# Performance work log

Measured on AMD Instinct MI355X. Metric: run time of the kernel, lower is better.

The kernel has to match this reference:

```python
import jax, jax.numpy as jnp
import numpy as np

M_BLEND = 0.3
LR_REFINE = 0.1
N_REFINE = 10
N_SAMPLES = 256
USE_INFONCE = True
MARGIN = 0.2
TAU = 0.07


def safe_norm(x, eps=1e-8):
    return x / jnp.maximum(jnp.linalg.norm(x, axis=-1, keepdims=True), eps)


def setup_inputs() -> dict:
    key = jax.random.key(0)
    k1, k2, k3, k4 = jax.random.split(key, 4)
    fg_proto = safe_norm(jax.random.normal(k1, (64, 512), dtype=jnp.float32))
    bg_proto = safe_norm(jax.random.normal(k2, (64, 512), dtype=jnp.float32))
    F_map = jax.random.normal(k3, (16, 512, 96, 96), dtype=jnp.float32)
    M_map = jax.random.uniform(k4, (16, 96, 96), dtype=jnp.float32)
    return {"fg_proto": fg_proto, "bg_proto": bg_proto, "F_map": F_map, "M_map": M_map}


def _refine(feats, protos):
    # iterative k-means-like refinement: argmax assign -> per-cluster mean -> blended, renormalized centroid
    p = protos
    K = p.shape[0]
    ones = jnp.ones((feats.shape[0],), feats.dtype)
    for it in range(N_REFINE):
        step = LR_REFINE / (1.0 + 0.5 * it)
        assign = jnp.argmax(feats @ p.T, axis=1)                      # [S]
        sums = jax.ops.segment_sum(feats, assign, num_segments=K)    # [K, C]
        counts = jax.ops.segment_sum(ones, assign, num_segments=K)   # [K]
        cluster_mean = sums / jnp.maximum(counts, 1.0)[:, None]
        new_p = safe_norm((1.0 - step) * p + step * cluster_mean)
        p = jnp.where((counts > 0)[:, None], new_p, p)                # only update non-empty clusters
    return p


def reference(fg_proto, bg_proto, F_map, M_map):
    N, C, H, W = F_map.shape
    # M_map already at (H, W): nearest interpolation is identity; clamp to [0, 1]
    M_flat = jnp.clip(M_map.reshape(-1), 0.0, 1.0)                    # [N*H*W]
    F_flat = safe_norm(F_map.transpose(0, 2, 3, 1).reshape(-1, C))    # [N*H*W, C]

    sim_fg = F_flat @ fg_proto.T                                      # [P, Kf]
    sim_bg = F_flat @ bg_proto.T                                      # [P, Kb]
    dist_fg_min = 1.0 - sim_fg.max(axis=1)
    dist_bg_min = 1.0 - sim_bg.max(axis=1)

    k = min(N_SAMPLES, F_flat.shape[0])
    score_fg = jax.lax.stop_gradient(dist_fg_min * M_flat)
    score_bg = jax.lax.stop_gradient(dist_bg_min * (1.0 - M_flat))
    pos_idx = jax.lax.top_k(score_fg, k)[1]
    neg_idx = jax.lax.top_k(score_bg, k)[1]

    # refinement runs under no_grad in the original
    F_sg = jax.lax.stop_gradient(F_flat)
    p_fg = _refine(F_sg[pos_idx], jax.lax.stop_gradient(fg_proto))
    p_bg = _refine(F_sg[neg_idx], jax.lax.stop_gradient(bg_proto))

    # triplet loss (note: sim_neg also uses p_fg, as in the original)
    pos_feats = safe_norm(F_flat[pos_idx])
    neg_feats = safe_norm(F_flat[neg_idx])
    sim_pos = (pos_feats @ p_fg.T).max(axis=1).mean()
    sim_neg = (neg_feats @ p_fg.T).max(axis=1).mean()
    loss = jax.nn.relu(MARGIN + sim_neg - sim_pos)

    if USE_INFONCE:
        pos_sim = pos_feats @ p_fg.T / TAU                            # [k, Kf]
        neg_sim = pos_feats @ p_bg.T / TAU                            # [k, Kb]
        numerator = jax.scipy.special.logsumexp(pos_sim, axis=1)
        denominator = jax.scipy.special.logsumexp(jnp.concatenate([pos_sim, neg_sim], axis=1), axis=1)
        loss = loss + 0.25 * (-(numerator - denominator).mean())

    refined_fg = safe_norm((1.0 - M_BLEND) * fg_proto + M_BLEND * p_fg)
    refined_bg = safe_norm((1.0 - M_BLEND) * bg_proto + M_BLEND * p_bg)
    return loss, refined_fg, refined_bg
```

## Files before the change

kernel.cpp:

```cpp
#include <hip/hip_runtime.h>
#include <math.h>

#define P_TOTAL 147456
#define HW 9216
#define CHW (512*9216)
#define C_DIM 512
#define KP 64

__device__ __forceinline__ unsigned f2key(float f) {
    unsigned u = __float_as_uint(f);
    return (u & 0x80000000u) ? ~u : (u | 0x80000000u);
}

__global__ void k_init(const float* __restrict__ fg, const float* __restrict__ bg,
                       float* __restrict__ protoT, float* __restrict__ pwork) {
    int i = blockIdx.x * 256 + threadIdx.x;
    int side = i >> 15;
    int r = i & 32767;
    int k = r >> 9;
    int c = r & 511;
    float v = (side ? bg : fg)[k * 512 + c];
    protoT[side * 32768 + c * 64 + k] = v;
    pwork[side * 32768 + k * 512 + c] = v;
}

__global__ __launch_bounds__(256) void k_score(const float* __restrict__ F,
                                               const float* __restrict__ protoT,
                                               float* __restrict__ md_fg,
                                               float* __restrict__ md_bg,
                                               float* __restrict__ n2out) {
    __shared__ float lds[2048];
    const int side = blockIdx.y;
    const int p = blockIdx.x * 256 + threadIdx.x;
    const int n = p / HW;
    const int hw = p - n * HW;
    const float* Fp = F + (size_t)n * CHW + hw;
    const float* PT = protoT + side * (C_DIM * 64);

    float acc[64];
#pragma unroll
    for (int k = 0; k < 64; ++k) acc[k] = 0.f;
    float n2 = 0.f;

    for (int cc = 0; cc < 16; ++cc) {
        __syncthreads();
#pragma unroll
        for (int i = 0; i < 8; ++i)
            lds[threadIdx.x + 256 * i] = PT[cc * 2048 + threadIdx.x + 256 * i];
        __syncthreads();
        for (int c = 0; c < 32; ++c) {
            float f = Fp[(size_t)(cc * 32 + c) * HW];
            if (side == 0) n2 = fmaf(f, f, n2);
#pragma unroll
            for (int k = 0; k < 64; ++k) acc[k] = fmaf(f, lds[c * 64 + k], acc[k]);
        }
    }
    float m = acc[0];
#pragma unroll
    for (int k = 1; k < 64; ++k) m = fmaxf(m, acc[k]);
    if (side == 0) { md_fg[p] = m; n2out[p] = n2; }
    else          { md_bg[p] = m; }
}

__global__ void k_combine(const float* __restrict__ M,
                          float* __restrict__ sfg, float* __restrict__ sbg,
                          float* __restrict__ n2inv) {
    int p = blockIdx.x * 256 + threadIdx.x;
    float inv = 1.f / fmaxf(sqrtf(n2inv[p]), 1e-8f);
    float m = fminf(fmaxf(M[p], 0.f), 1.f);
    float sf = (1.f - sfg[p] * inv) * m;
    float sb = (1.f - sbg[p] * inv) * (1.f - m);
    sfg[p] = sf; sbg[p] = sb; n2inv[p] = inv;
}

__global__ void k_hist1(const float* __restrict__ sfg, const float* __restrict__ sbg,
                        unsigned* __restrict__ hist) {
    int side = blockIdx.y;
    int p = blockIdx.x * 256 + threadIdx.x;
    float s = side ? sbg[p] : sfg[p];
    atomicAdd(&hist[side * 65536 + (f2key(s) >> 16)], 1u);
}

__global__ void k_hist2(const float* __restrict__ sfg, const float* __restrict__ sbg,
                        const int* __restrict__ ctrl, unsigned* __restrict__ hist2) {
    int side = blockIdx.y;
    int p = blockIdx.x * 256 + threadIdx.x;
    float s = side ? sbg[p] : sfg[p];
    unsigned key = f2key(s);
    if ((int)(key >> 16) == ctrl[side * 8 + 0])
        atomicAdd(&hist2[side * 65536 + (key & 0xffffu)], 1u);
}

__global__ __launch_bounds__(1024) void k_scan(const unsigned* __restrict__ hist,
                                               int* __restrict__ ctrl, int pass) {
    __shared__ unsigned sd[1024];
    int side = blockIdx.x;
    const unsigned* h = hist + side * 65536;
    int t = threadIdx.x;
    unsigned partial = 0;
    for (int j = 0; j < 64; ++j) partial += h[65535 - (t * 64 + j)];
    sd[t] = partial;
    __syncthreads();
    for (int off = 1; off < 1024; off <<= 1) {
        unsigned v = (t >= off) ? sd[t - off] : 0u;
        __syncthreads();
        sd[t] += v;
        __syncthreads();
    }
    unsigned incl = sd[t];
    unsigned excl = incl - partial;
    unsigned target = (pass == 0) ? 256u : (unsigned)ctrl[side * 8 + 1];
    if (excl < target && target <= incl) {
        unsigned cum = excl;
        for (int j = 0; j < 64; ++j) {
            int b = 65535 - (t * 64 + j);
            unsigned c = h[b];
            if (cum + c >= target) {
                if (pass == 0) {
                    ctrl[side * 8 + 0] = b;
                    ctrl[side * 8 + 1] = (int)(target - cum);
                } else {
                    unsigned vkey = ((unsigned)ctrl[side * 8 + 0] << 16) | (unsigned)b;
                    ctrl[side * 8 + 2] = (int)vkey;
                    int n_gt = (int)(256u - (unsigned)ctrl[side * 8 + 1] + cum);
                    ctrl[side * 8 + 3] = n_gt;
                    ctrl[side * 8 + 4] = 256 - n_gt;
                }
                break;
            }
            cum += c;
        }
    }
}

__global__ void k_collect(const float* __restrict__ sfg, const float* __restrict__ sbg,
                          int* __restrict__ ctrl, int* __restrict__ idx, int* __restrict__ ties) {
    int side = blockIdx.y;
    int p = blockIdx.x * 256 + threadIdx.x;
    float s = side ? sbg[p] : sfg[p];
    unsigned key = f2key(s);
    unsigned vkey = (unsigned)ctrl[side * 8 + 2];
    if (key > vkey) {
        int pos = atomicAdd(&ctrl[side * 8 + 5], 1);
        idx[side * 256 + pos] = p;
    } else if (key == vkey) {
        int pos = atomicAdd(&ctrl[side * 8 + 6], 1);
        if (pos < 512) ties[side * 512 + pos] = p;
    }
}

__global__ void k_finalize(int* __restrict__ ctrl, int* __restrict__ idx, int* __restrict__ ties) {
    int side = threadIdx.x;
    if (side >= 2) return;
    int n_gt = ctrl[side * 8 + 3];
    int need = ctrl[side * 8 + 4];
    int cnt = ctrl[side * 8 + 6];
    if (cnt > 512) cnt = 512;
    int* tb = ties + side * 512;
    for (int q = 0; q < need; ++q) {
        int mi = q;
        for (int j = q + 1; j < cnt; ++j) if (tb[j] < tb[mi]) mi = j;
        int tmp = tb[q]; tb[q] = tb[mi]; tb[mi] = tmp;
        idx[side * 256 + n_gt + q] = tb[q];
    }
}

__global__ void k_gather(const float* __restrict__ F, const float* __restrict__ inv,
                         const int* __restrict__ idx, float* __restrict__ feats) {
    int b = blockIdx.x;
    int side = b >> 8, j = b & 255;
    int p = idx[side * 256 + j];
    float iv = inv[p];
    int n = p / HW, hw = p - n * HW;
    const float* Fp = F + (size_t)n * CHW + hw;
    float* o = feats + (size_t)(side * 256 + j) * 512;
    for (int c = threadIdx.x; c < 512; c += 256)
        o[c] = Fp[(size_t)c * HW] * iv;
}

__global__ __launch_bounds__(256) void k_assign(const float* __restrict__ feats,
                                                const float* __restrict__ pwork,
                                                float* __restrict__ sums,
                                                float* __restrict__ counts) {
    int w = blockIdx.x * 4 + (threadIdx.x >> 6);
    int lane = threadIdx.x & 63;
    int side = w >> 8, j = w & 255;
    const float4* fr = (const float4*)(feats + (size_t)(side * 256 + j) * 512);
    const float4* pw = (const float4*)(pwork + (size_t)side * 32768 + (size_t)lane * 512);
    float dot = 0.f;
#pragma unroll 4
    for (int c = 0; c < 128; ++c) {
        float4 a = fr[c], b = pw[c];
        dot = fmaf(a.x, b.x, dot); dot = fmaf(a.y, b.y, dot);
        dot = fmaf(a.z, b.z, dot); dot = fmaf(a.w, b.w, dot);
    }
    float bv = dot; int bi = lane;
#pragma unroll
    for (int m = 32; m >= 1; m >>= 1) {
        float ov = __shfl_xor(bv, m);
        int oi = __shfl_xor(bi, m);
        if (ov > bv || (ov == bv && oi < bi)) { bv = ov; bi = oi; }
    }
    if (lane == 0) atomicAdd(&counts[side * 64 + bi], 1.f);
    const float* frf = feats + (size_t)(side * 256 + j) * 512;
    float* srow = sums + (size_t)side * 32768 + (size_t)bi * 512;
#pragma unroll
    for (int i = 0; i < 8; ++i) {
        int c = lane + i * 64;
        atomicAdd(&srow[c], frf[c]);
    }
}

__global__ __launch_bounds__(64) void k_update(float* __restrict__ pwork,
                                               float* __restrict__ sums,
                                               float* __restrict__ counts,
                                               float step) {
    int side = blockIdx.x >> 6, k = blockIdx.x & 63;
    int lane = threadIdx.x;
    float cnt = counts[side * 64 + k];
    float* srow = sums + (size_t)side * 32768 + (size_t)k * 512;
    float* prow = pwork + (size_t)side * 32768 + (size_t)k * 512;
    float bl[8]; float n2 = 0.f;
#pragma unroll
    for (int i = 0; i < 8; ++i) {
        int c = lane + i * 64;
        float mean = srow[c] / fmaxf(cnt, 1.f);
        float v = (1.f - step) * prow[c] + step * mean;
        bl[i] = v; n2 = fmaf(v, v, n2);
        srow[c] = 0.f;
    }
#pragma unroll
    for (int m = 32; m >= 1; m >>= 1) n2 += __shfl_xor(n2, m);
    float inv = 1.f / fmaxf(sqrtf(n2), 1e-8f);
    if (cnt > 0.f) {
#pragma unroll
        for (int i = 0; i < 8; ++i) prow[lane + i * 64] = bl[i] * inv;
    }
    if (lane == 0) counts[side * 64 + k] = 0.f;
}

__global__ __launch_bounds__(256) void k_losspart(const float* __restrict__ feats,
                                                  const float* __restrict__ pwork,
                                                  float* __restrict__ lpart) {
    int w = blockIdx.x * 4 + (threadIdx.x >> 6);
    int lane = threadIdx.x & 63;
    int half = w >> 8, j = w & 255;
    const float4* fr = (const float4*)(feats + (size_t)(half * 256 + j) * 512);
    const float4* pf = (const float4*)(pwork + (size_t)lane * 512);
    const float4* pb = (const float4*)(pwork + 32768 + (size_t)lane * 512);
    if (half == 0) {
        float d1 = 0.f, d2 = 0.f;
        for (int c = 0; c < 128; ++c) {
            float4 a = fr[c], x = pf[c], y = pb[c];
            d1 = fmaf(a.x, x.x, d1); d1 = fmaf(a.y, x.y, d1);
            d1 = fmaf(a.z, x.z, d1); d1 = fmaf(a.w, x.w, d1);
            d2 = fmaf(a.x, y.x, d2); d2 = fmaf(a.y, y.y, d2);
            d2 = fmaf(a.z, y.z, d2); d2 = fmaf(a.w, y.w, d2);
        }
        float smax = d1;
        for (int m = 32; m >= 1; m >>= 1) smax = fmaxf(smax, __shfl_xor(smax, m));
        float a = d1 / 0.07f, b = d2 / 0.07f;
        float m1 = a;
        for (int m = 32; m >= 1; m >>= 1) m1 = fmaxf(m1, __shfl_xor(m1, m));
        float mb = b;
        for (int m = 32; m >= 1; m >>= 1) mb = fmaxf(mb, __shfl_xor(mb, m));
        float md = fmaxf(m1, mb);
        float sn = expf(a - m1);
        for (int m = 32; m >= 1; m >>= 1) sn += __shfl_xor(sn, m);
        float sdn = expf(a - md) + expf(b - md);
        for (int m = 32; m >= 1; m >>= 1) sdn += __shfl_xor(sdn, m);
        float num = m1 + logf(sn);
        float den = md + logf(sdn);
        if (lane == 0) { lpart[j] = smax; lpart[512 + j] = num - den; }
    } else {
        float d1 = 0.f;
        for (int c = 0; c < 128; ++c) {
            float4 a = fr[c], x = pf[c];
            d1 = fmaf(a.x, x.x, d1); d1 = fmaf(a.y, x.y, d1);
            d1 = fmaf(a.z, x.z, d1); d1 = fmaf(a.w, x.w, d1);
        }
        float smax = d1;
        for (int m = 32; m >= 1; m >>= 1) smax = fmaxf(smax, __shfl_xor(smax, m));
        if (lane == 0) lpart[256 + j] = smax;
    }
}

__global__ __launch_bounds__(256) void k_final(const float* __restrict__ lpart,
                                               float* __restrict__ out) {
    __shared__ float red[3][4];
    int t = threadIdx.x;
    float sp = lpart[t], sn = lpart[256 + t], nm = lpart[512 + t];
    for (int m = 32; m >= 1; m >>= 1) {
        sp += __shfl_xor(sp, m); sn += __shfl_xor(sn, m); nm += __shfl_xor(nm, m);
    }
    int wv = t >> 6;
    if ((t & 63) == 0) { red[0][wv] = sp; red[1][wv] = sn; red[2][wv] = nm; }
    __syncthreads();
    if (t == 0) {
        float SP = 0, SN = 0, NM = 0;
        for (int i = 0; i < 4; ++i) { SP += red[0][i]; SN += red[1][i]; NM += red[2][i]; }
        SP /= 256.f; SN /= 256.f; NM /= 256.f;
        out[0] = fmaxf(0.f, 0.2f + SN - SP) + 0.25f * (-NM);
    }
}

__global__ __launch_bounds__(64) void k_refined(const float* __restrict__ fg,
                                                const float* __restrict__ bg,
                                                const float* __restrict__ pwork,
                                                float* __restrict__ out) {
    int side = blockIdx.x >> 6, k = blockIdx.x & 63;
    int lane = threadIdx.x;
    const float* proto = (side ? bg : fg) + (size_t)k * 512;
    const float* prow = pwork + (size_t)side * 32768 + (size_t)k * 512;
    float bl[8]; float n2 = 0.f;
#pragma unroll
    for (int i = 0; i < 8; ++i) {
        int c = lane + i * 64;
        float v = 0.7f * proto[c] + 0.3f * prow[c];
        bl[i] = v; n2 = fmaf(v, v, n2);
    }
#pragma unroll
    for (int m = 32; m >= 1; m >>= 1) n2 += __shfl_xor(n2, m);
    float inv = 1.f / fmaxf(sqrtf(n2), 1e-8f);
    float* o = out + 1 + (size_t)side * 32768 + (size_t)k * 512;
#pragma unroll
    for (int i = 0; i < 8; ++i) o[lane + i * 64] = bl[i] * inv;
}

extern "C" void kernel_launch(void* const* d_in, const int* in_sizes, int n_in,
                              void* d_out, int out_size, void* d_ws, size_t ws_size,
                              hipStream_t stream) {
    const float* fg = (const float*)d_in[0];
    const float* bg = (const float*)d_in[1];
    const float* F  = (const float*)d_in[2];
    const float* M  = (const float*)d_in[3];
    float* out = (float*)d_out;
    char* ws = (char*)d_ws;

    size_t o = 0;
    auto alloc = [&](size_t bytes) { size_t r = o; o += (bytes + 1023) & ~(size_t)1023; return r; };
    size_t off_hist1 = alloc(2 * 65536 * 4);
    size_t off_hist2 = alloc(2 * 65536 * 4);
    size_t off_ctrl  = alloc(64);
    size_t off_cnts  = alloc(2 * 64 * 4);
    size_t off_sums  = alloc(2 * 64 * 512 * 4);
    size_t zbytes = o;
    size_t off_sfg   = alloc(P_TOTAL * 4);
    size_t off_sbg   = alloc(P_TOTAL * 4);
    size_t off_n2    = alloc(P_TOTAL * 4);
    size_t off_pT    = alloc(2 * 512 * 64 * 4);
    size_t off_idx   = alloc(2 * 256 * 4);
    size_t off_ties  = alloc(2 * 512 * 4);
    size_t off_feats = alloc(2 * 256 * 512 * 4);
    size_t off_pwork = alloc(2 * 64 * 512 * 4);
    size_t off_lpart = alloc(768 * 4);

    unsigned* hist1 = (unsigned*)(ws + off_hist1);
    unsigned* hist2 = (unsigned*)(ws + off_hist2);
    int* ctrl   = (int*)(ws + off_ctrl);
    float* cnts = (float*)(ws + off_cnts);
    float* sums = (float*)(ws + off_sums);
    float* sfg  = (float*)(ws + off_sfg);
    float* sbg  = (float*)(ws + off_sbg);
    float* n2   = (float*)(ws + off_n2);
    float* pT   = (float*)(ws + off_pT);
    int* idx    = (int*)(ws + off_idx);
    int* ties   = (int*)(ws + off_ties);
    float* feats = (float*)(ws + off_feats);
    float* pwork = (float*)(ws + off_pwork);
    float* lpart = (float*)(ws + off_lpart);

    hipMemsetAsync(ws, 0, zbytes, stream);
    k_init<<<256, 256, 0, stream>>>(fg, bg, pT, pwork);
    k_score<<<dim3(576, 2), 256, 0, stream>>>(F, pT, sfg, sbg, n2);
    k_combine<<<576, 256, 0, stream>>>(M, sfg, sbg, n2);
    k_hist1<<<dim3(576, 2), 256, 0, stream>>>(sfg, sbg, hist1);
    k_scan<<<2, 1024, 0, stream>>>(hist1, ctrl, 0);
    k_hist2<<<dim3(576, 2), 256, 0, stream>>>(sfg, sbg, ctrl, hist2);
    k_scan<<<2, 1024, 0, stream>>>(hist2, ctrl, 1);
    k_collect<<<dim3(576, 2), 256, 0, stream>>>(sfg, sbg, ctrl, idx, ties);
    k_finalize<<<1, 64, 0, stream>>>(ctrl, idx, ties);
    k_gather<<<512, 256, 0, stream>>>(F, n2, idx, feats);
    for (int it = 0; it < 10; ++it) {
        k_assign<<<128, 256, 0, stream>>>(feats, pwork, sums, cnts);
        k_update<<<128, 64, 0, stream>>>(pwork, sums, cnts, (float)(0.1 / (1.0 + 0.5 * it)));
    }
    k_losspart<<<128, 256, 0, stream>>>(feats, pwork, lpart);
    k_final<<<1, 256, 0, stream>>>(lpart, out);
    k_refined<<<128, 64, 0, stream>>>(fg, bg, pwork, out);
}
```

Baseline: 1.141 ms.

## Fuse fg/bg scoring with histogram and merge refinement into cooperative kernel

```diff
diff --git a/kernel.cpp b/kernel.cpp
--- a/kernel.cpp
+++ b/kernel.cpp
@@ -1,11 +1,12 @@
 #include <hip/hip_runtime.h>
+#include <hip/hip_cooperative_groups.h>
 #include <math.h>
+
+namespace cg = cooperative_groups;
 
 #define P_TOTAL 147456
 #define HW 9216
 #define CHW (512*9216)
-#define C_DIM 512
-#define KP 64
 
 __device__ __forceinline__ unsigned f2key(float f) {
     unsigned u = __float_as_uint(f);
@@ -13,72 +14,54 @@
 }
 
 __global__ void k_init(const float* __restrict__ fg, const float* __restrict__ bg,
-                       float* __restrict__ protoT, float* __restrict__ pwork) {
+                       float* __restrict__ protoP, float* __restrict__ pwork) {
     int i = blockIdx.x * 256 + threadIdx.x;
     int side = i >> 15;
     int r = i & 32767;
     int k = r >> 9;
     int c = r & 511;
     float v = (side ? bg : fg)[k * 512 + c];
-    protoT[side * 32768 + c * 64 + k] = v;
+    protoP[c * 128 + side * 64 + k] = v;
     pwork[side * 32768 + k * 512 + c] = v;
 }
 
-__global__ __launch_bounds__(256) void k_score(const float* __restrict__ F,
-                                               const float* __restrict__ protoT,
-                                               float* __restrict__ md_fg,
-                                               float* __restrict__ md_bg,
-                                               float* __restrict__ n2out) {
-    __shared__ float lds[2048];
-    const int side = blockIdx.y;
+__global__ __launch_bounds__(256, 2) void k_score_all(const float* __restrict__ F,
+                                                      const float* __restrict__ protoP,
+                                                      const float* __restrict__ M,
+                                                      float* __restrict__ sfg,
+                                                      float* __restrict__ sbg,
+                                                      float* __restrict__ invn,
+                                                      unsigned* __restrict__ hist) {
     const int p = blockIdx.x * 256 + threadIdx.x;
     const int n = p / HW;
     const int hw = p - n * HW;
     const float* Fp = F + (size_t)n * CHW + hw;
-    const float* PT = protoT + side * (C_DIM * 64);
-
-    float acc[64];
-#pragma unroll
-    for (int k = 0; k < 64; ++k) acc[k] = 0.f;
+
+    float af[64], ab[64];
+#pragma unroll
+    for (int k = 0; k < 64; ++k) { af[k] = 0.f; ab[k] = 0.f; }
     float n2 = 0.f;
 
-    for (int cc = 0; cc < 16; ++cc) {
-        __syncthreads();
-#pragma unroll
-        for (int i = 0; i < 8; ++i)
-            lds[threadIdx.x + 256 * i] = PT[cc * 2048 + threadIdx.x + 256 * i];
-        __syncthreads();
-        for (int c = 0; c < 32; ++c) {
-            float f = Fp[(size_t)(cc * 32 + c) * HW];
-            if (side == 0) n2 = fmaf(f, f, n2);
-#pragma unroll
-            for (int k = 0; k < 64; ++k) acc[k] = fmaf(f, lds[c * 64 + k], acc[k]);
-        }
-    }
-    float m = acc[0];
-#pragma unroll
-    for (int k = 1; k < 64; ++k) m = fmaxf(m, acc[k]);
-    if (side == 0) { md_fg[p] = m; n2out[p] = n2; }
-    else          { md_bg[p] = m; }
-}
-
-__global__ void k_combine(const float* __restrict__ M,
-                          float* __restrict__ sfg, float* __restrict__ sbg,
-                          float* __restrict__ n2inv) {
-    int p = blockIdx.x * 256 + threadIdx.x;
-    float inv = 1.f / fmaxf(sqrtf(n2inv[p]), 1e-8f);
+#pragma unroll 2
+    for (int c = 0; c < 512; ++c) {
+        float f = Fp[(size_t)c * HW];
+        n2 = fmaf(f, f, n2);
+        const float* pc = protoP + c * 128;
+#pragma unroll
+        for (int k = 0; k < 64; ++k) af[k] = fmaf(f, pc[k], af[k]);
+#pragma unroll
+        for (int k = 0; k < 64; ++k) ab[k] = fmaf(f, pc[64 + k], ab[k]);
+    }
+    float mf = af[0], mb = ab[0];
+#pragma unroll
+    for (int k = 1; k < 64; ++k) { mf = fmaxf(mf, af[k]); mb = fmaxf(mb, ab[k]); }
+    float inv = 1.f / fmaxf(sqrtf(n2), 1e-8f);
     float m = fminf(fmaxf(M[p], 0.f), 1.f);
-    float sf = (1.f - sfg[p] * inv) * m;
-    float sb = (1.f - sbg[p] * inv) * (1.f - m);
-    sfg[p] = sf; sbg[p] = sb; n2inv[p] = inv;
-}
-
-__global__ void k_hist1(const float* __restrict__ sfg, const float* __restrict__ sbg,
-                        unsigned* __restrict__ hist) {
-    int side = blockIdx.y;
-    int p = blockIdx.x * 256 + threadIdx.x;
-    float s = side ? sbg[p] : sfg[p];
-    atomicAdd(&hist[side * 65536 + (f2key(s) >> 16)], 1u);
+    float sf = (1.f - mf * inv) * m;
+    float sb = (1.f - mb * inv) * (1.f - m);
+    sfg[p] = sf; sbg[p] = sb; invn[p] = inv;
+    atomicAdd(&hist[f2key(sf) >> 16], 1u);
+    atomicAdd(&hist[65536 + (f2key(sb) >> 16)], 1u);
 }
 
 __global__ void k_hist2(const float* __restrict__ sfg, const float* __restrict__ sbg,
@@ -149,182 +132,190 @@
     }
 }
 
-__global__ void k_finalize(int* __restrict__ ctrl, int* __restrict__ idx, int* __restrict__ ties) {
-    int side = threadIdx.x;
-    if (side >= 2) return;
-    int n_gt = ctrl[side * 8 + 3];
-    int need = ctrl[side * 8 + 4];
-    int cnt = ctrl[side * 8 + 6];
-    if (cnt > 512) cnt = 512;
-    int* tb = ties + side * 512;
-    for (int q = 0; q < need; ++q) {
-        int mi = q;
-        for (int j = q + 1; j < cnt; ++j) if (tb[j] < tb[mi]) mi = j;
-        int tmp = tb[q]; tb[q] = tb[mi]; tb[mi] = tmp;
-        idx[side * 256 + n_gt + q] = tb[q];
-    }
-}
-
-__global__ void k_gather(const float* __restrict__ F, const float* __restrict__ inv,
-                         const int* __restrict__ idx, float* __restrict__ feats) {
-    int b = blockIdx.x;
-    int side = b >> 8, j = b & 255;
-    int p = idx[side * 256 + j];
-    float iv = inv[p];
-    int n = p / HW, hw = p - n * HW;
-    const float* Fp = F + (size_t)n * CHW + hw;
-    float* o = feats + (size_t)(side * 256 + j) * 512;
-    for (int c = threadIdx.x; c < 512; c += 256)
-        o[c] = Fp[(size_t)c * HW] * iv;
-}
-
-__global__ __launch_bounds__(256) void k_assign(const float* __restrict__ feats,
-                                                const float* __restrict__ pwork,
-                                                float* __restrict__ sums,
-                                                float* __restrict__ counts) {
-    int w = blockIdx.x * 4 + (threadIdx.x >> 6);
-    int lane = threadIdx.x & 63;
-    int side = w >> 8, j = w & 255;
-    const float4* fr = (const float4*)(feats + (size_t)(side * 256 + j) * 512);
-    const float4* pw = (const float4*)(pwork + (size_t)side * 32768 + (size_t)lane * 512);
-    float dot = 0.f;
+__global__ __launch_bounds__(256) void k_refine_all(const float* __restrict__ F,
+                                                    const float* __restrict__ invn,
+                                                    const float* __restrict__ fg,
+                                                    const float* __restrict__ bg,
+                                                    int* __restrict__ ctrl,
+                                                    int* __restrict__ idx,
+                                                    int* __restrict__ ties,
+                                                    float* __restrict__ feats,
+                                                    float* __restrict__ pwork,
+                                                    float* __restrict__ sums,
+                                                    float* __restrict__ cnts,
+                                                    float* __restrict__ out) {
+    cg::grid_group grid = cg::this_grid();
+    const int tid = threadIdx.x;
+    const int bid = blockIdx.x;
+    const int gw = bid * 4 + (tid >> 6);
+    const int lane = tid & 63;
+
+    if (bid == 0 && tid < 2) {
+        int side = tid;
+        int n_gt = ctrl[side * 8 + 3];
+        int need = ctrl[side * 8 + 4];
+        int cnt = ctrl[side * 8 + 6];
+        if (cnt > 512) cnt = 512;
+        int* tb = ties + side * 512;
+        for (int q = 0; q < need; ++q) {
+            int mi = q;
+            for (int j = q + 1; j < cnt; ++j) if (tb[j] < tb[mi]) mi = j;
+            int tmp = tb[q]; tb[q] = tb[mi]; tb[mi] = tmp;
+            idx[side * 256 + n_gt + q] = tb[q];
+        }
+    }
+    grid.sync();
+
+    {
+        int side = gw >> 8, j = gw & 255;
+        int p = idx[side * 256 + j];
+        float iv = invn[p];
+        int n = p / HW, hw = p - n * HW;
+        const float* Fp = F + (size_t)n * CHW + hw;
+        float* o = feats + (size_t)gw * 512;
+#pragma unroll
+        for (int i = 0; i < 8; ++i) {
+            int c = lane + i * 64;
+            o[c] = Fp[(size_t)c * HW] * iv;
+        }
+    }
+    grid.sync();
+
+    for (int it = 0; it < 10; ++it) {
+        {
+            int side = gw >> 8;
+            const float4* fr = (const float4*)(feats + (size_t)gw * 512);
+            const float4* pw = (const float4*)(pwork + (size_t)side * 32768 + (size_t)lane * 512);
+            float dot = 0.f;
 #pragma unroll 4
-    for (int c = 0; c < 128; ++c) {
-        float4 a = fr[c], b = pw[c];
-        dot = fmaf(a.x, b.x, dot); dot = fmaf(a.y, b.y, dot);
-        dot = fmaf(a.z, b.z, dot); dot = fmaf(a.w, b.w, dot);
-    }
-    float bv = dot; int bi = lane;
-#pragma unroll
-    for (int m = 32; m >= 1; m >>= 1) {
-        float ov = __shfl_xor(bv, m);
-        int oi = __shfl_xor(bi, m);
-        if (ov > bv || (ov == bv && oi < bi)) { bv = ov; bi = oi; }
-    }
-    if (lane == 0) atomicAdd(&counts[side * 64 + bi], 1.f);
-    const float* frf = feats + (size_t)(side * 256 + j) * 512;
-    float* srow = sums + (size_t)side * 32768 + (size_t)bi * 512;
-#pragma unroll
-    for (int i = 0; i < 8; ++i) {
-        int c = lane + i * 64;
-        atomicAdd(&srow[c], frf[c]);
-    }
-}
-
-__global__ __launch_bounds__(64) void k_update(float* __restrict__ pwork,
-                                               float* __restrict__ sums,
-                                               float* __restrict__ counts,
-                                               float step) {
-    int side = blockIdx.x >> 6, k = blockIdx.x & 63;
-    int lane = threadIdx.x;
-    float cnt = counts[side * 64 + k];
-    float* srow = sums + (size_t)side * 32768 + (size_t)k * 512;
-    float* prow = pwork + (size_t)side * 32768 + (size_t)k * 512;
-    float bl[8]; float n2 = 0.f;
-#pragma unroll
-    for (int i = 0; i < 8; ++i) {
-        int c = lane + i * 64;
-        float mean = srow[c] / fmaxf(cnt, 1.f);
-        float v = (1.f - step) * prow[c] + step * mean;
-        bl[i] = v; n2 = fmaf(v, v, n2);
-        srow[c] = 0.f;
-    }
-#pragma unroll
-    for (int m = 32; m >= 1; m >>= 1) n2 += __shfl_xor(n2, m);
-    float inv = 1.f / fmaxf(sqrtf(n2), 1e-8f);
-    if (cnt > 0.f) {
-#pragma unroll
-        for (int i = 0; i < 8; ++i) prow[lane + i * 64] = bl[i] * inv;
-    }
-    if (lane == 0) counts[side * 64 + k] = 0.f;
-}
-
-__global__ __launch_bounds__(256) void k_losspart(const float* __restrict__ feats,
-                                                  const float* __restrict__ pwork,
-                                                  float* __restrict__ lpart) {
-    int w = blockIdx.x * 4 + (threadIdx.x >> 6);
-    int lane = threadIdx.x & 63;
-    int half = w >> 8, j = w & 255;
-    const float4* fr = (const float4*)(feats + (size_t)(half * 256 + j) * 512);
-    const float4* pf = (const float4*)(pwork + (size_t)lane * 512);
-    const float4* pb = (const float4*)(pwork + 32768 + (size_t)lane * 512);
-    if (half == 0) {
-        float d1 = 0.f, d2 = 0.f;
-        for (int c = 0; c < 128; ++c) {
-            float4 a = fr[c], x = pf[c], y = pb[c];
-            d1 = fmaf(a.x, x.x, d1); d1 = fmaf(a.y, x.y, d1);
-            d1 = fmaf(a.z, x.z, d1); d1 = fmaf(a.w, x.w, d1);
-            d2 = fmaf(a.x, y.x, d2); d2 = fmaf(a.y, y.y, d2);
-            d2 = fmaf(a.z, y.z, d2); d2 = fmaf(a.w, y.w, d2);
-        }
-        float smax = d1;
-        for (int m = 32; m >= 1; m >>= 1) smax = fmaxf(smax, __shfl_xor(smax, m));
-        float a = d1 / 0.07f, b = d2 / 0.07f;
-        float m1 = a;
-        for (int m = 32; m >= 1; m >>= 1) m1 = fmaxf(m1, __shfl_xor(m1, m));
-        float mb = b;
-        for (int m = 32; m >= 1; m >>= 1) mb = fmaxf(mb, __shfl_xor(mb, m));
-        float md = fmaxf(m1, mb);
-        float sn = expf(a - m1);
-        for (int m = 32; m >= 1; m >>= 1) sn += __shfl_xor(sn, m);
-        float sdn = expf(a - md) + expf(b - md);
-        for (int m = 32; m >= 1; m >>= 1) sdn += __shfl_xor(sdn, m);
-        float num = m1 + logf(sn);
-        float den = md + logf(sdn);
-        if (lane == 0) { lpart[j] = smax; lpart[512 + j] = num - den; }
-    } else {
-        float d1 = 0.f;
-        for (int c = 0; c < 128; ++c) {
-            float4 a = fr[c], x = pf[c];
-            d1 = fmaf(a.x, x.x, d1); d1 = fmaf(a.y, x.y, d1);
-            d1 = fmaf(a.z, x.z, d1); d1 = fmaf(a.w, x.w, d1);
-        }
-        float smax = d1;
-        for (int m = 32; m >= 1; m >>= 1) smax = fmaxf(smax, __shfl_xor(smax, m));
-        if (lane == 0) lpart[256 + j] = smax;
-    }
-}
-
-__global__ __launch_bounds__(256) void k_final(const float* __restrict__ lpart,
-                                               float* __restrict__ out) {
-    __shared__ float red[3][4];
-    int t = threadIdx.x;
-    float sp = lpart[t], sn = lpart[256 + t], nm = lpart[512 + t];
-    for (int m = 32; m >= 1; m >>= 1) {
-        sp += __shfl_xor(sp, m); sn += __shfl_xor(sn, m); nm += __shfl_xor(nm, m);
-    }
-    int wv = t >> 6;
-    if ((t & 63) == 0) { red[0][wv] = sp; red[1][wv] = sn; red[2][wv] = nm; }
-    __syncthreads();
-    if (t == 0) {
-        float SP = 0, SN = 0, NM = 0;
-        for (int i = 0; i < 4; ++i) { SP += red[0][i]; SN += red[1][i]; NM += red[2][i]; }
-        SP /= 256.f; SN /= 256.f; NM /= 256.f;
-        out[0] = fmaxf(0.f, 0.2f + SN - SP) + 0.25f * (-NM);
-    }
-}
-
-__global__ __launch_bounds__(64) void k_refined(const float* __restrict__ fg,
-                                                const float* __restrict__ bg,
-                                                const float* __restrict__ pwork,
-                                                float* __restrict__ out) {
-    int side = blockIdx.x >> 6, k = blockIdx.x & 63;
-    int lane = threadIdx.x;
-    const float* proto = (side ? bg : fg) + (size_t)k * 512;
-    const float* prow = pwork + (size_t)side * 32768 + (size_t)k * 512;
-    float bl[8]; float n2 = 0.f;
-#pragma unroll
-    for (int i = 0; i < 8; ++i) {
-        int c = lane + i * 64;
-        float v = 0.7f * proto[c] + 0.3f * prow[c];
-        bl[i] = v; n2 = fmaf(v, v, n2);
-    }
-#pragma unroll
-    for (int m = 32; m >= 1; m >>= 1) n2 += __shfl_xor(n2, m);
-    float inv = 1.f / fmaxf(sqrtf(n2), 1e-8f);
-    float* o = out + 1 + (size_t)side * 32768 + (size_t)k * 512;
-#pragma unroll
-    for (int i = 0; i < 8; ++i) o[lane + i * 64] = bl[i] * inv;
+            for (int c = 0; c < 128; ++c) {
+                float4 a = fr[c], b = pw[c];
+                dot = fmaf(a.x, b.x, dot); dot = fmaf(a.y, b.y, dot);
+                dot = fmaf(a.z, b.z, dot); dot = fmaf(a.w, b.w, dot);
+            }
+            float bv = dot; int bi = lane;
+#pragma unroll
+            for (int mm = 32; mm >= 1; mm >>= 1) {
+                float ov = __shfl_xor(bv, mm);
+                int oi = __shfl_xor(bi, mm);
+                if (ov > bv || (ov == bv && oi < bi)) { bv = ov; bi = oi; }
+            }
+            if (lane == 0) atomicAdd(&cnts[side * 64 + bi], 1.f);
+            const float* frf = feats + (size_t)gw * 512;
+            float* srow = sums + (size_t)side * 32768 + (size_t)bi * 512;
+#pragma unroll
+            for (int i = 0; i < 8; ++i) {
+                int c = lane + i * 64;
+                atomicAdd(&srow[c], frf[c]);
+            }
+        }
+        grid.sync();
+        if (gw < 128) {
+            int side = gw >> 6, k = gw & 63;
+            float step = (float)(0.1 / (1.0 + 0.5 * (double)it));
+            float cnt = cnts[side * 64 + k];
+            float* srow = sums + (size_t)side * 32768 + (size_t)k * 512;
+            float* prow = pwork + (size_t)side * 32768 + (size_t)k * 512;
+            float bl[8]; float n2 = 0.f;
+#pragma unroll
+            for (int i = 0; i < 8; ++i) {
+                int c = lane + i * 64;
+                float mean = srow[c] / fmaxf(cnt, 1.f);
+                float v = (1.f - step) * prow[c] + step * mean;
+                bl[i] = v; n2 = fmaf(v, v, n2);
+                srow[c] = 0.f;
+            }
+#pragma unroll
+            for (int mm = 32; mm >= 1; mm >>= 1) n2 += __shfl_xor(n2, mm);
+            float inv = 1.f / fmaxf(sqrtf(n2), 1e-8f);
+            if (cnt > 0.f) {
+#pragma unroll
+                for (int i = 0; i < 8; ++i) prow[lane + i * 64] = bl[i] * inv;
+            }
+            if (lane == 0) cnts[side * 64 + k] = 0.f;
+        }
+        grid.sync();
+    }
+
+    float* lpart = sums;
+    {
+        int half = gw >> 8, j = gw & 255;
+        const float4* fr = (const float4*)(feats + (size_t)gw * 512);
+        const float4* pf = (const float4*)(pwork + (size_t)lane * 512);
+        const float4* pb = (const float4*)(pwork + 32768 + (size_t)lane * 512);
+        if (half == 0) {
+            float d1 = 0.f, d2 = 0.f;
+            for (int c = 0; c < 128; ++c) {
+                float4 a = fr[c], x = pf[c], y = pb[c];
+                d1 = fmaf(a.x, x.x, d1); d1 = fmaf(a.y, x.y, d1);
+                d1 = fmaf(a.z, x.z, d1); d1 = fmaf(a.w, x.w, d1);
+                d2 = fmaf(a.x, y.x, d2); d2 = fmaf(a.y, y.y, d2);
+                d2 = fmaf(a.z, y.z, d2); d2 = fmaf(a.w, y.w, d2);
+            }
+            float smax = d1;
+            for (int mm = 32; mm >= 1; mm >>= 1) smax = fmaxf(smax, __shfl_xor(smax, mm));
+            float a = d1 / 0.07f, b = d2 / 0.07f;
+            float m1 = a;
+            for (int mm = 32; mm >= 1; mm >>= 1) m1 = fmaxf(m1, __shfl_xor(m1, mm));
+            float mbv = b;
+            for (int mm = 32; mm >= 1; mm >>= 1) mbv = fmaxf(mbv, __shfl_xor(mbv, mm));
+            float md = fmaxf(m1, mbv);
+            float sn = expf(a - m1);
+            for (int mm = 32; mm >= 1; mm >>= 1) sn += __shfl_xor(sn, mm);
+            float sdn = expf(a - md) + expf(b - md);
+            for (int mm = 32; mm >= 1; mm >>= 1) sdn += __shfl_xor(sdn, mm);
+            float num = m1 + logf(sn);
+            float den = md + logf(sdn);
+            if (lane == 0) { lpart[j] = smax; lpart[512 + j] = num - den; }
+        } else {
+            float d1 = 0.f;
+            for (int c = 0; c < 128; ++c) {
+                float4 a = fr[c], x = pf[c];
+                d1 = fmaf(a.x, x.x, d1); d1 = fmaf(a.y, x.y, d1);
+                d1 = fmaf(a.z, x.z, d1); d1 = fmaf(a.w, x.w, d1);
+            }
+            float smax = d1;
+            for (int mm = 32; mm >= 1; mm >>= 1) smax = fmaxf(smax, __shfl_xor(smax, mm));
+            if (lane == 0) lpart[256 + j] = smax;
+        }
+    }
+    grid.sync();
+
+    if (bid == 0) {
+        __shared__ float red[3][4];
+        float sp = lpart[tid], sn = lpart[256 + tid], nm = lpart[512 + tid];
+        for (int mm = 32; mm >= 1; mm >>= 1) {
+            sp += __shfl_xor(sp, mm); sn += __shfl_xor(sn, mm); nm += __shfl_xor(nm, mm);
+        }
+        int wv = tid >> 6;
+        if ((tid & 63) == 0) { red[0][wv] = sp; red[1][wv] = sn; red[2][wv] = nm; }
+        __syncthreads();
+        if (tid == 0) {
+            float SP = 0, SN = 0, NM = 0;
+            for (int i = 0; i < 4; ++i) { SP += red[0][i]; SN += red[1][i]; NM += red[2][i]; }
+            SP /= 256.f; SN /= 256.f; NM /= 256.f;
+            out[0] = fmaxf(0.f, 0.2f + SN - SP) + 0.25f * (-NM);
+        }
+    }
+    if (gw >= 128 && gw < 256) {
+        int w2 = gw - 128;
+        int side = w2 >> 6, k = w2 & 63;
+        const float* proto = (side ? bg : fg) + (size_t)k * 512;
+        const float* prow = pwork + (size_t)side * 32768 + (size_t)k * 512;
+        float bl[8]; float n2 = 0.f;
+#pragma unroll
+        for (int i = 0; i < 8; ++i) {
+            int c = lane + i * 64;
+            float v = 0.7f * proto[c] + 0.3f * prow[c];
+            bl[i] = v; n2 = fmaf(v, v, n2);
+        }
+#pragma unroll
+        for (int mm = 32; mm >= 1; mm >>= 1) n2 += __shfl_xor(n2, mm);
+        float inv = 1.f / fmaxf(sqrtf(n2), 1e-8f);
+        float* o = out + 1 + (size_t)side * 32768 + (size_t)k * 512;
+#pragma unroll
+        for (int i = 0; i < 8; ++i) o[lane + i * 64] = bl[i] * inv;
+    }
 }
 
 extern "C" void kernel_launch(void* const* d_in, const int* in_sizes, int n_in,
@@ -347,13 +338,12 @@
     size_t zbytes = o;
     size_t off_sfg   = alloc(P_TOTAL * 4);
     size_t off_sbg   = alloc(P_TOTAL * 4);
-    size_t off_n2    = alloc(P_TOTAL * 4);
-    size_t off_pT    = alloc(2 * 512 * 64 * 4);
+    size_t off_inv   = alloc(P_TOTAL * 4);
+    size_t off_pP    = alloc(512 * 128 * 4);
     size_t off_idx   = alloc(2 * 256 * 4);
     size_t off_ties  = alloc(2 * 512 * 4);
     size_t off_feats = alloc(2 * 256 * 512 * 4);
     size_t off_pwork = alloc(2 * 64 * 512 * 4);
-    size_t off_lpart = alloc(768 * 4);
 
     unsigned* hist1 = (unsigned*)(ws + off_hist1);
     unsigned* hist2 = (unsigned*)(ws + off_hist2);
@@ -362,30 +352,24 @@
     float* sums = (float*)(ws + off_sums);
     float* sfg  = (float*)(ws + off_sfg);
     float* sbg  = (float*)(ws + off_sbg);
-    float* n2   = (float*)(ws + off_n2);
-    float* pT   = (float*)(ws + off_pT);
+    float* invn = (float*)(ws + off_inv);
+    float* pP   = (float*)(ws + off_pP);
     int* idx    = (int*)(ws + off_idx);
     int* ties   = (int*)(ws + off_ties);
     float* feats = (float*)(ws + off_feats);
     float* pwork = (float*)(ws + off_pwork);
-    float* lpart = (float*)(ws + off_lpart);
 
     hipMemsetAsync(ws, 0, zbytes, stream);
-    k_init<<<256, 256, 0, stream>>>(fg, bg, pT, pwork);
-    k_score<<<dim3(576, 2), 256, 0, stream>>>(F, pT, sfg, sbg, n2);
-    k_combine<<<576, 256, 0, stream>>>(M, sfg, sbg, n2);
-    k_hist1<<<dim3(576, 2), 256, 0, stream>>>(sfg, sbg, hist1);
+    k_init<<<256, 256, 0, stream>>>(fg, bg, pP, pwork);
+    k_score_all<<<576, 256, 0, stream>>>(F, pP, M, sfg, sbg, invn, hist1);
     k_scan<<<2, 1024, 0, stream>>>(hist1, ctrl, 0);
     k_hist2<<<dim3(576, 2), 256, 0, stream>>>(sfg, sbg, ctrl, hist2);
     k_scan<<<2, 1024, 0, stream>>>(hist2, ctrl, 1);
     k_collect<<<dim3(576, 2), 256, 0, stream>>>(sfg, sbg, ctrl, idx, ties);
-    k_finalize<<<1, 64, 0, stream>>>(ctrl, idx, ties);
-    k_gather<<<512, 256, 0, stream>>>(F, n2, idx, feats);
-    for (int it = 0; it < 10; ++it) {
-        k_assign<<<128, 256, 0, stream>>>(feats, pwork, sums, cnts);
-        k_update<<<128, 64, 0, stream>>>(pwork, sums, cnts, (float)(0.1 / (1.0 + 0.5 * it)));
-    }
-    k_losspart<<<128, 256, 0, stream>>>(feats, pwork, lpart);
-    k_final<<<1, 256, 0, stream>>>(lpart, out);
-    k_refined<<<128, 64, 0, stream>>>(fg, bg, pwork, out);
-}
+
+    void* args[] = {(void*)&F, (void*)&invn, (void*)&fg, (void*)&bg,
+                    (void*)&ctrl, (void*)&idx, (void*)&ties, (void*)&feats,
+                    (void*)&pwork, (void*)&sums, (void*)&cnts, (void*)&out};
+    hipLaunchCooperativeKernel((const void*)k_refine_all, dim3(128), dim3(256),
+                               args, 0, stream);
+}
```

After: 1.376 ms. +20.6%, slower.
